# Kernel tuning notes

Hardware: AMD Instinct MI355X
Metric: run time of the kernel (lower is better)

The kernel has to match this reference:

```python
import jax, jax.numpy as jnp
import numpy as np

NUM_HEADS = 12


def setup_inputs() -> dict:
    key = jax.random.key(0)
    k_x, k_m, k_qkv, k_proj = jax.random.split(key, 4)
    B, N, C = 2, 2048, 768
    x = jax.random.normal(k_x, (B, N, C), dtype=jnp.float32)
    # binary key mask: 1 = attend, 0 = masked out
    mask = jax.random.randint(k_m, (B, N), 0, 2).astype(jnp.int32)
    # torch Linear(dim, dim*3, bias=False): stored here as [in, out]
    w_qkv = jax.random.normal(k_qkv, (C, 3 * C), dtype=jnp.float32) * 0.02
    w_proj = jax.random.normal(k_proj, (C, C), dtype=jnp.float32) * 0.02
    b_proj = jnp.zeros((C,), dtype=jnp.float32)
    return {"x": x, "mask": mask, "w_qkv": w_qkv, "w_proj": w_proj, "b_proj": b_proj}


def reference(x, mask, w_qkv, w_proj, b_proj):
    B, N, C = x.shape
    H = NUM_HEADS
    hd = C // H
    scale = hd ** -0.5
    qkv = (x @ w_qkv).reshape(B, N, 3, H, hd)
    q, k, v = jnp.moveaxis(qkv, 2, 0)            # each [B, N, H, hd]
    attn = jnp.einsum('bnhd,bmhd->bhnm', q, k) * scale  # [B, H, N, N]
    # faithful masked_softmax: unstable exp (no max subtraction), mask keys, renormalize
    m = mask.astype(x.dtype)[:, None, None, :]   # [B, 1, 1, N]
    x_exp = jnp.exp(attn) * m
    attn = x_exp / x_exp.sum(-1, keepdims=True)
    out = jnp.einsum('bhnm,bmhd->bnhd', attn, v).reshape(B, N, C)
    return out @ w_proj + b_proj
```

## Files before the change

### kernel.cpp

```cpp
#include <hip/hip_runtime.h>
#include <cstdint>

#define NB 2
#define NSEQ 2048
#define CDIM 768
#define NH 12
#define HD 64
#define NTOK (NB*NSEQ)
#define QKV_COLS (3*CDIM)
#define NBLK ((NSEQ/64)*NH*NB)

typedef short bf16x8 __attribute__((ext_vector_type(8)));
typedef short bf16x4 __attribute__((ext_vector_type(4)));
typedef float f32x4  __attribute__((ext_vector_type(4)));
typedef short short4v __attribute__((ext_vector_type(4)));
typedef unsigned int uint2v __attribute__((ext_vector_type(2)));
typedef unsigned int uint4v __attribute__((ext_vector_type(4)));

#define MFMA16(a,b,c) __builtin_amdgcn_mfma_f32_16x16x32_bf16(a,b,c,0,0,0)

__device__ __forceinline__ short f2b(float f) {
    uint32_t u = __builtin_bit_cast(uint32_t, f);
    u += 0x7fffu + ((u >> 16) & 1u);
    return (short)(u >> 16);
}
__device__ __forceinline__ unsigned pack2(float a, float b) {
    unsigned ua = __builtin_bit_cast(unsigned, a) + 0x7fffu;
    unsigned ub = __builtin_bit_cast(unsigned, b) + 0x7fffu;
    return __builtin_amdgcn_perm(ub, ua, 0x07060302u);
}
__device__ __forceinline__ void gll16(const short* g, short* l) {
    __builtin_amdgcn_global_load_lds(
        (const __attribute__((address_space(1))) unsigned int*)g,
        (__attribute__((address_space(3))) unsigned int*)l, 16, 0, 0);
}

__global__ __launch_bounds__(256) void prep_kernel(
    const float* __restrict__ x, const float* __restrict__ w_qkv,
    const float* __restrict__ w_proj,
    short* __restrict__ xb, short* __restrict__ wqt, short* __restrict__ wpt)
{
    __shared__ float tile[32][33];
    const int bid = blockIdx.x, t = threadIdx.x;
    if (bid < 3072) {
        int i = bid * 256 + t;
        float4 v = ((const float4*)x)[i];
        short4v o = { f2b(v.x), f2b(v.y), f2b(v.z), f2b(v.w) };
        ((short4v*)xb)[i] = o;
        return;
    }
    const float* w; short* wt; int K, NC, n0, k0;
    if (bid < 3072 + 1728) {
        int r = bid - 3072;
        w = w_qkv; wt = wqt; K = CDIM; NC = QKV_COLS;
        n0 = (r % 72) * 32; k0 = (r / 72) * 32;
    } else {
        int r = bid - 4800;
        w = w_proj; wt = wpt; K = CDIM; NC = CDIM;
        n0 = (r % 24) * 32; k0 = (r / 24) * 32;
    }
    #pragma unroll
    for (int i = 0; i < 4; ++i) {
        int idx = t + i * 256; int r = idx >> 5, c = idx & 31;
        tile[r][c] = w[(size_t)(k0 + r) * NC + n0 + c];
    }
    __syncthreads();
    #pragma unroll
    for (int i = 0; i < 4; ++i) {
        int idx = t + i * 256; int r = idx >> 5, c = idx & 31;
        wt[(size_t)(n0 + r) * K + k0 + c] = f2b(tile[c][r]);
    }
}

#define STAGEG(K0, B) do {                                                       \
    short* a_ = As + (B)*4096; short* b_ = Bs + (B)*4096;                        \
    gll16(ag0 + (K0), a_ + wid*512);                                             \
    gll16(ag1 + (K0), a_ + 2048 + wid*512);                                      \
    gll16(bg0 + (K0), b_ + wid*512);                                             \
    gll16(bg1 + (K0), b_ + 2048 + wid*512);                                      \
} while (0)

#define COMPUTEG(B) do {                                                         \
    const short* A_ = As + (B)*4096; const short* B_ = Bs + (B)*4096;            \
    bf16x8 af_[4], bf_[4];                                                       \
    _Pragma("unroll")                                                            \
    for (int i = 0; i < 4; ++i)                                                  \
        af_[i] = *(const bf16x8*)&A_[(wA*64 + i*16 + l16) * 32 + quad*8];        \
    _Pragma("unroll")                                                            \
    for (int j = 0; j < 4; ++j)                                                  \
        bf_[j] = *(const bf16x8*)&B_[(wB*64 + j*16 + l16) * 32 + quad*8];        \
    _Pragma("unroll")                                                            \
    for (int i = 0; i < 4; ++i)                                                  \
        _Pragma("unroll")                                                        \
        for (int j = 0; j < 4; ++j)                                              \
            acc[i][j] = MFMA16(af_[i], bf_[j], acc[i][j]);                       \
} while (0)

#define GEMM_LOOP() do {                                                         \
    STAGEG(0, 0); __syncthreads();                                               \
    for (int k0 = 0; k0 < CDIM; k0 += 64) {                                      \
        STAGEG(k0 + 32, 1);                                                      \
        COMPUTEG(0);                                                             \
        __syncthreads();                                                         \
        STAGEG((k0 + 64 < CDIM) ? k0 + 64 : 0, 0);                               \
        COMPUTEG(1);                                                             \
        __syncthreads();                                                         \
    }                                                                            \
} while (0)

__global__ __launch_bounds__(256) void gemm_qkv(
    const short* __restrict__ A ,
    const short* __restrict__ B ,
    short* __restrict__ qb, short* __restrict__ kb, short* __restrict__ vt)
{
    __shared__ short As[8192];
    __shared__ short Bs[8192];
    const int t = threadIdx.x;
    const int lane = t & 63, wid = t >> 6;
    const int quad = lane >> 4, l16 = lane & 15;
    const int wA = wid >> 1, wB = wid & 1;
    const int n0 = blockIdx.x * 128;
    const int m0 = blockIdx.y * 128;

    const int srow = wid * 16 + (lane >> 2), schunk = (lane & 3) * 8;
    const short* ag0 = A + (size_t)(n0 + srow) * CDIM + schunk;
    const short* ag1 = ag0 + (size_t)64 * CDIM;
    const short* bg0 = B + (size_t)(m0 + srow) * CDIM + schunk;
    const short* bg1 = bg0 + (size_t)64 * CDIM;

    f32x4 acc[4][4] = {};
    GEMM_LOOP();

    const int colbase = n0 + wA * 64;
    const int s = colbase / CDIM;
    const int h = (colbase - s * CDIM) >> 6;
    const int b = m0 >> 11;
    const size_t bh = (size_t)(b * NH + h);
    const float qsc = (s == 0) ? 0.125f : 1.0f;
    #pragma unroll
    for (int i = 0; i < 4; ++i) {
        const int d0 = i*16 + quad*4;
        #pragma unroll
        for (int j = 0; j < 4; ++j) {
            int tok = (m0 + wB*64 + j*16 + l16) & (NSEQ - 1);
            if (s < 2) {
                short* dst = (s == 0 ? qb : kb) + (bh * NSEQ + tok) * HD + d0;
                short4v o = { f2b(acc[i][j][0] * qsc), f2b(acc[i][j][1] * qsc),
                              f2b(acc[i][j][2] * qsc), f2b(acc[i][j][3] * qsc) };
                *(short4v*)dst = o;
            } else {
                short* dst = vt + (bh * HD + d0) * NSEQ + tok;
                #pragma unroll
                for (int r = 0; r < 4; ++r)
                    dst[(size_t)r * NSEQ] = f2b(acc[i][j][r]);
            }
        }
    }
}

#define STAGE64(KT, BUF) do {                                                    \
    short* kd_ = (BUF);                                                          \
    short* vd_ = (BUF) + 4096;                                                   \
    _Pragma("unroll")                                                            \
    for (int j = 0; j < 2; ++j) {                                                \
        gll16(kp + (size_t)((KT) + sRow[j]) * HD + sC[j]*8, kd_ + wid*1024 + j*512); \
        gll16(vp + (size_t)sRow[j] * NSEQ + (KT) + sC[j]*8, vd_ + wid*1024 + j*512); \
    }                                                                            \
} while (0)

#define BODY_S(KT, BUF, pP, vL) do {                                             \
    const short* Kb_ = (BUF);                                                    \
    const short* Vb_ = (BUF) + 4096;                                             \
    int4 mi_ = *(const int4*)(mp + (KT) + kbase);                                \
    bf16x8 kf0_ = *(const bf16x8*)&Kb_[krow64 + kc0];                            \
    bf16x8 kf1_ = *(const bf16x8*)&Kb_[krow64 + kc1];                            \
    f32x4 s_[4] = {};                                                            \
    _Pragma("unroll")                                                            \
    for (int jt = 0; jt < 4; ++jt) {                                             \
        s_[jt] = MFMA16(kf0_, qf[jt][0], s_[jt]);                                \
        s_[jt] = MFMA16(kf1_, qf[jt][1], s_[jt]);                                \
    }                                                                            \
    float4 m_ = {(float)mi_.x, (float)mi_.y, (float)mi_.z, (float)mi_.w};        \
    _Pragma("unroll")                                                            \
    for (int jt = 0; jt < 4; ++jt) {                                             \
        float e0 = __expf(s_[jt][0]) * m_.x;                                     \
        float e1 = __expf(s_[jt][1]) * m_.y;                                     \
        float e2 = __expf(s_[jt][2]) * m_.z;                                     \
        float e3 = __expf(s_[jt][3]) * m_.w;                                     \
        l[jt] += (e0 + e1) + (e2 + e3);                                          \
        pP[jt] = (uint2v){ pack2(e0, e1), pack2(e2, e3) };                       \
    }                                                                            \
    _Pragma("unroll")                                                            \
    for (int it = 0; it < 4; ++it)                                               \
        vL[it] = *(const bf16x4*)&Vb_[(it*16 + l16)*64 + vslot + vsub];          \
} while (0)

#define BODY_PV(pLo, vLo, pHi, vHi) do {                                         \
    bf16x8 pb_[4];                                                               \
    _Pragma("unroll")                                                            \
    for (int jt = 0; jt < 4; ++jt) {                                             \
        uint4v u_ = { pLo[jt].x, pLo[jt].y, pHi[jt].x, pHi[jt].y };              \
        pb_[jt] = __builtin_bit_cast(bf16x8, u_);                                \
    }                                                                            \
    _Pragma("unroll")                                                            \
    for (int it = 0; it < 4; ++it) {                                             \
        bf16x8 vf_ = __builtin_shufflevector(vLo[it], vHi[it], 0,1,2,3,4,5,6,7); \
        _Pragma("unroll")                                                        \
        for (int jt = 0; jt < 4; ++jt)                                           \
            o_acc[it][jt] = MFMA16(vf_, pb_[jt], o_acc[it][jt]);                 \
    }                                                                            \
} while (0)

__global__ __launch_bounds__(256) void attn_kernel(
    const short* __restrict__ qb, const short* __restrict__ kb,
    const short* __restrict__ vt, const int* __restrict__ mask,
    short* __restrict__ ao)
{
    __shared__ __align__(16) short KV2[2][8192];
    float (*Ob)[68] = (float(*)[68])KV2;
    float (*lsum)[64] = (float(*)[64])((char*)KV2 + 17408);

    const int t = threadIdx.x;
    const int lane = t & 63, wid = t >> 6;
    const int quad = lane >> 4, l16 = lane & 15;
    const int id = blockIdx.x;
    const int idx = id >> 3;
    const int bh = (id & 7) + ((idx % 3) << 3);
    const int q0 = (idx / 3) << 6;
    const int b = bh / NH, h = bh - b * NH;
    const size_t hoff = (size_t)bh * NSEQ * HD;
    const short* qp = qb + hoff;
    const short* kp = kb + hoff;
    const short* vp = vt + hoff;
    const int* mp = mask + b * NSEQ;
    const int kbase = wid * 16 + quad * 4;

    int sRow[2], sC[2];
    #pragma unroll
    for (int j = 0; j < 2; ++j) {
        sRow[j] = wid * 16 + j * 8 + (lane >> 3);
        sC[j]   = (lane & 7) ^ (sRow[j] & 7);
    }
    const int r7 = l16 & 7;
    const int krow64 = (wid * 16 + l16) * 64;
    const int kc0 = ((quad       ^ r7) << 3);
    const int kc1 = (((quad + 4) ^ r7) << 3);
    const int vslot = (((wid*2 + (quad >> 1)) ^ r7) << 3);
    const int vsub  = (quad & 1) * 4;

    bf16x8 qf[4][2];
    #pragma unroll
    for (int jt = 0; jt < 4; ++jt) {
        const short* qr = qp + (size_t)(q0 + jt*16 + l16) * HD + quad*8;
        qf[jt][0] = *(const bf16x8*)qr;
        qf[jt][1] = *(const bf16x8*)(qr + 32);
    }

    f32x4 o_acc[4][4] = {};
    float l[4] = {0.f, 0.f, 0.f, 0.f};
    uint2v pLo[4], pHi[4];
    bf16x4 vLo[4], vHi[4];

    STAGE64(0, KV2[0]);
    __syncthreads();

    for (int kt = 0; kt < NSEQ; kt += 128) {
        STAGE64(kt + 64, KV2[1]);
        BODY_S(kt, KV2[0], pLo, vLo);
        __syncthreads();
        STAGE64((kt + 128) & (NSEQ - 1), KV2[0]);
        BODY_S(kt + 64, KV2[1], pHi, vHi);
        BODY_PV(pLo, vLo, pHi, vHi);
        __syncthreads();
    }

    #pragma unroll
    for (int jt = 0; jt < 4; ++jt) {
        l[jt] += __shfl_xor(l[jt], 16);
        l[jt] += __shfl_xor(l[jt], 32);
        if (quad == 0) lsum[wid][jt*16 + l16] = l[jt];
    }
    for (int w = 0; w < 4; ++w) {
        __syncthreads();
        if (wid == w) {
            #pragma unroll
            for (int it = 0; it < 4; ++it)
                #pragma unroll
                for (int jt = 0; jt < 4; ++jt)
                    #pragma unroll
                    for (int r = 0; r < 4; ++r) {
                        if (w == 0)
                            Ob[it*16 + quad*4 + r][jt*16 + l16] = o_acc[it][jt][r];
                        else
                            Ob[it*16 + quad*4 + r][jt*16 + l16] += o_acc[it][jt][r];
                    }
        }
    }
    __syncthreads();

    {
        const int ql = t >> 2, dc = (t & 3) * 16;
        float inv = 1.0f / (((lsum[0][ql] + lsum[1][ql]) +
                             (lsum[2][ql] + lsum[3][ql])));
        bf16x8 o8a, o8b;
        #pragma unroll
        for (int d = 0; d < 8; ++d) o8a[d] = f2b(Ob[dc + d][ql] * inv);
        #pragma unroll
        for (int d = 0; d < 8; ++d) o8b[d] = f2b(Ob[dc + 8 + d][ql] * inv);
        int tok = b * NSEQ + q0 + ql;
        short* dst = ao + (size_t)tok * CDIM + h * HD + dc;
        *(bf16x8*)dst = o8a;
        *(bf16x8*)(dst + 8) = o8b;
    }
}

__global__ __launch_bounds__(256) void gemm_proj(
    const short* __restrict__ A ,
    const short* __restrict__ B ,
    const float* __restrict__ bias, float* __restrict__ out)
{
    __shared__ short As[8192];
    __shared__ short Bs[8192];
    const int t = threadIdx.x;
    const int lane = t & 63, wid = t >> 6;
    const int quad = lane >> 4, l16 = lane & 15;
    const int wA = wid >> 1, wB = wid & 1;
    const int n0 = blockIdx.x * 128;
    const int m0 = blockIdx.y * 128;

    const int srow = wid * 16 + (lane >> 2), schunk = (lane & 3) * 8;
    const short* ag0 = A + (size_t)(n0 + srow) * CDIM + schunk;
    const short* ag1 = ag0 + (size_t)64 * CDIM;
    const short* bg0 = B + (size_t)(m0 + srow) * CDIM + schunk;
    const short* bg1 = bg0 + (size_t)64 * CDIM;

    f32x4 acc[4][4] = {};
    GEMM_LOOP();

    #pragma unroll
    for (int i = 0; i < 4; ++i) {
        int col0 = n0 + wA*64 + i*16 + quad*4;
        float4 bias4 = *(const float4*)&bias[col0];
        #pragma unroll
        for (int j = 0; j < 4; ++j) {
            int tok = m0 + wB*64 + j*16 + l16;
            float4 o = { acc[i][j][0] + bias4.x, acc[i][j][1] + bias4.y,
                         acc[i][j][2] + bias4.z, acc[i][j][3] + bias4.w };
            *(float4*)(out + (size_t)tok * CDIM + col0) = o;
        }
    }
}

extern "C" void kernel_launch(void* const* d_in, const int* in_sizes, int n_in,
                              void* d_out, int out_size, void* d_ws, size_t ws_size,
                              hipStream_t stream)
{
    const float* x      = (const float*)d_in[0];
    const int*   mask   = (const int*)d_in[1];
    const float* w_qkv  = (const float*)d_in[2];
    const float* w_proj = (const float*)d_in[3];
    const float* b_proj = (const float*)d_in[4];
    float* out = (float*)d_out;

    const size_t SZ = (size_t)NTOK * CDIM;
    short* xb  = (short*)d_ws;
    short* wqt = xb  + SZ;
    short* wpt = wqt + (size_t)QKV_COLS * CDIM;
    short* qb  = wpt + (size_t)CDIM * CDIM;
    short* kb  = qb  + SZ;
    short* vt  = kb  + SZ;
    short* ao  = vt  + SZ;

    dim3 blk(256);
    prep_kernel<<<dim3(5376), blk, 0, stream>>>(x, w_qkv, w_proj, xb, wqt, wpt);
    gemm_qkv<<<dim3(QKV_COLS/128, NTOK/128), blk, 0, stream>>>(wqt, xb, qb, kb, vt);
    attn_kernel<<<dim3(NBLK), blk, 0, stream>>>(qb, kb, vt, mask, ao);
    gemm_proj<<<dim3(CDIM/128, NTOK/128), blk, 0, stream>>>(wpt, ao, b_proj, out);
}
```

Baseline: 181.3 us.

## Split attention over key halves with a reduce kernel; stage QKV epilogue through LDS

The attention kernel now splits each query tile's key range into two halves. This doubles the block count from 768 to 1536 to fill more CUs. Each half writes unnormalized fp32 partial outputs and row sums, and a new reduce kernel combines them and normalizes to bf16. Separately, the QKV GEMM epilogue transposes its tile through shared memory so Q/K/V stores become coalesced 16-byte writes instead of scattered short writes. The cost is extra fp32 partial traffic, an additional kernel launch, and an extra barrier in the GEMM epilogue.

```diff
diff --git a/kernel.cpp b/kernel.cpp
--- a/kernel.cpp
+++ b/kernel.cpp
@@ -8,7 +8,8 @@
 #define HD 64
 #define NTOK (NB*NSEQ)
 #define QKV_COLS (3*CDIM)
-#define NBLK ((NSEQ/64)*NH*NB)
+#define NBLK_ATTN (((NSEQ/64)*NH*NB)*2)
+#define NBLK_RED  ((NSEQ/64)*NH*NB)
 
 typedef short bf16x8 __attribute__((ext_vector_type(8)));
 typedef short bf16x4 __attribute__((ext_vector_type(4)));
@@ -113,8 +114,9 @@
     const short* __restrict__ B ,
     short* __restrict__ qb, short* __restrict__ kb, short* __restrict__ vt)
 {
-    __shared__ short As[8192];
-    __shared__ short Bs[8192];
+    __shared__ __align__(16) short SM[17408];
+    short* const As = SM;
+    short* const Bs = SM + 8192;
     const int t = threadIdx.x;
     const int lane = t & 63, wid = t >> 6;
     const int quad = lane >> 4, l16 = lane & 15;
@@ -131,30 +133,51 @@
     f32x4 acc[4][4] = {};
     GEMM_LOOP();
 
-    const int colbase = n0 + wA * 64;
-    const int s = colbase / CDIM;
-    const int h = (colbase - s * CDIM) >> 6;
-    const int b = m0 >> 11;
-    const size_t bh = (size_t)(b * NH + h);
+    const int s  = n0 / CDIM;
+    const int h0 = (n0 - s * CDIM) >> 6;
+    const int b  = m0 >> 11;
     const float qsc = (s == 0) ? 0.125f : 1.0f;
-    #pragma unroll
-    for (int i = 0; i < 4; ++i) {
-        const int d0 = i*16 + quad*4;
-        #pragma unroll
-        for (int j = 0; j < 4; ++j) {
-            int tok = (m0 + wB*64 + j*16 + l16) & (NSEQ - 1);
-            if (s < 2) {
-                short* dst = (s == 0 ? qb : kb) + (bh * NSEQ + tok) * HD + d0;
-                short4v o = { f2b(acc[i][j][0] * qsc), f2b(acc[i][j][1] * qsc),
-                              f2b(acc[i][j][2] * qsc), f2b(acc[i][j][3] * qsc) };
-                *(short4v*)dst = o;
-            } else {
-                short* dst = vt + (bh * HD + d0) * NSEQ + tok;
+    short* const CT = SM;
+
+    if (s < 2) {
+        #pragma unroll
+        for (int i = 0; i < 4; ++i)
+            #pragma unroll
+            for (int j = 0; j < 4; ++j) {
+                int tok = wB*64 + j*16 + l16;
+                int col = wA*64 + i*16 + quad*4;
+                short4v o = { f2b(acc[i][j][0]*qsc), f2b(acc[i][j][1]*qsc),
+                              f2b(acc[i][j][2]*qsc), f2b(acc[i][j][3]*qsc) };
+                *(short4v*)&CT[tok*136 + col] = o;
+            }
+        __syncthreads();
+        const int tok = t >> 1, hf = t & 1;
+        short* dst = (s == 0 ? qb : kb)
+                   + ((size_t)(b*NH + h0 + hf) * NSEQ + (m0 & 2047) + tok) * HD;
+        const short* src = &CT[tok*136 + hf*64];
+        #pragma unroll
+        for (int k = 0; k < 8; ++k)
+            *(float4*)(dst + k*8) = *(const float4*)(src + k*8);
+    } else {
+        #pragma unroll
+        for (int i = 0; i < 4; ++i)
+            #pragma unroll
+            for (int j = 0; j < 4; ++j) {
+                int tok = wB*64 + j*16 + l16;
+                int col = wA*64 + i*16 + quad*4;
                 #pragma unroll
                 for (int r = 0; r < 4; ++r)
-                    dst[(size_t)r * NSEQ] = f2b(acc[i][j][r]);
+                    CT[(col + r)*136 + tok] = f2b(acc[i][j][r]);
             }
-        }
+        __syncthreads();
+        const int row = t >> 1, hf = t & 1;
+        const int hh = h0 + (row >> 6), d = row & 63;
+        short* dst = vt + ((size_t)(b*NH + hh) * HD + d) * NSEQ
+                   + (m0 & 2047) + hf*64;
+        const short* src = &CT[row*136 + hf*64];
+        #pragma unroll
+        for (int k = 0; k < 8; ++k)
+            *(float4*)(dst + k*8) = *(const float4*)(src + k*8);
     }
 }
 
@@ -214,7 +237,7 @@
 __global__ __launch_bounds__(256) void attn_kernel(
     const short* __restrict__ qb, const short* __restrict__ kb,
     const short* __restrict__ vt, const int* __restrict__ mask,
-    short* __restrict__ ao)
+    float* __restrict__ opart, float* __restrict__ lpart)
 {
     __shared__ __align__(16) short KV2[2][8192];
     float (*Ob)[68] = (float(*)[68])KV2;
@@ -226,7 +249,10 @@
     const int id = blockIdx.x;
     const int idx = id >> 3;
     const int bh = (id & 7) + ((idx % 3) << 3);
-    const int q0 = (idx / 3) << 6;
+    const int rem = idx / 3;
+    const int q0 = (rem >> 1) << 6;
+    const int split = rem & 1;
+    const int koff = split << 10;
     const int b = bh / NH, h = bh - b * NH;
     const size_t hoff = (size_t)bh * NSEQ * HD;
     const short* qp = qb + hoff;
@@ -234,6 +260,7 @@
     const short* vp = vt + hoff;
     const int* mp = mask + b * NSEQ;
     const int kbase = wid * 16 + quad * 4;
+    const int slab = ((bh * 32 + (q0 >> 6)) << 1) + split;
 
     int sRow[2], sC[2];
     #pragma unroll
@@ -261,14 +288,14 @@
     uint2v pLo[4], pHi[4];
     bf16x4 vLo[4], vHi[4];
 
-    STAGE64(0, KV2[0]);
+    STAGE64(koff, KV2[0]);
     __syncthreads();
 
-    for (int kt = 0; kt < NSEQ; kt += 128) {
+    for (int kt = koff; kt < koff + 1024; kt += 128) {
         STAGE64(kt + 64, KV2[1]);
         BODY_S(kt, KV2[0], pLo, vLo);
         __syncthreads();
-        STAGE64((kt + 128) & (NSEQ - 1), KV2[0]);
+        STAGE64((kt + 128 < koff + 1024) ? kt + 128 : koff, KV2[0]);
         BODY_S(kt + 64, KV2[1], pHi, vHi);
         BODY_PV(pLo, vLo, pHi, vHi);
         __syncthreads();
@@ -300,18 +327,49 @@
 
     {
         const int ql = t >> 2, dc = (t & 3) * 16;
-        float inv = 1.0f / (((lsum[0][ql] + lsum[1][ql]) +
-                             (lsum[2][ql] + lsum[3][ql])));
-        bf16x8 o8a, o8b;
-        #pragma unroll
-        for (int d = 0; d < 8; ++d) o8a[d] = f2b(Ob[dc + d][ql] * inv);
-        #pragma unroll
-        for (int d = 0; d < 8; ++d) o8b[d] = f2b(Ob[dc + 8 + d][ql] * inv);
-        int tok = b * NSEQ + q0 + ql;
-        short* dst = ao + (size_t)tok * CDIM + h * HD + dc;
-        *(bf16x8*)dst = o8a;
-        *(bf16x8*)(dst + 8) = o8b;
-    }
+        float* po = opart + (size_t)slab * 4096 + ql * 64 + dc;
+        #pragma unroll
+        for (int k = 0; k < 4; ++k) {
+            float4 o4 = { Ob[dc + k*4 + 0][ql], Ob[dc + k*4 + 1][ql],
+                          Ob[dc + k*4 + 2][ql], Ob[dc + k*4 + 3][ql] };
+            *(float4*)(po + k*4) = o4;
+        }
+        if (t < 64)
+            lpart[(size_t)slab * 64 + t] =
+                ((lsum[0][t] + lsum[1][t]) + (lsum[2][t] + lsum[3][t]));
+    }
+}
+
+__global__ __launch_bounds__(256) void attn_reduce(
+    const float* __restrict__ opart, const float* __restrict__ lpart,
+    short* __restrict__ ao)
+{
+    const int id = blockIdx.x, t = threadIdx.x;
+    const int xcd = id & 7, g = id >> 3;
+    const int qt = g & 31, bhhi = g >> 5;
+    const int bh = xcd + (bhhi << 3);
+    const int b = bh / NH, h = bh - b * NH;
+    const int slab0 = (bh * 32 + qt) << 1;
+    const int ql = t >> 2, dc = (t & 3) << 4;
+    const float* p0 = opart + (size_t)slab0 * 4096 + ql * 64 + dc;
+    const float* p1 = p0 + 4096;
+    const float inv = 1.0f /
+        (lpart[(size_t)slab0 * 64 + ql] + lpart[(size_t)(slab0 + 1) * 64 + ql]);
+    bf16x8 oa, ob;
+    #pragma unroll
+    for (int k = 0; k < 2; ++k) {
+        float4 a0 = ((const float4*)p0)[k*2],     a1 = ((const float4*)p0)[k*2+1];
+        float4 c0 = ((const float4*)p1)[k*2],     c1 = ((const float4*)p1)[k*2+1];
+        bf16x8 o8;
+        o8[0] = f2b((a0.x + c0.x) * inv); o8[1] = f2b((a0.y + c0.y) * inv);
+        o8[2] = f2b((a0.z + c0.z) * inv); o8[3] = f2b((a0.w + c0.w) * inv);
+        o8[4] = f2b((a1.x + c1.x) * inv); o8[5] = f2b((a1.y + c1.y) * inv);
+        o8[6] = f2b((a1.z + c1.z) * inv); o8[7] = f2b((a1.w + c1.w) * inv);
+        if (k == 0) oa = o8; else ob = o8;
+    }
+    short* dst = ao + ((size_t)(b * NSEQ + qt * 64 + ql)) * CDIM + h * HD + dc;
+    *(bf16x8*)dst = oa;
+    *(bf16x8*)(dst + 8) = ob;
 }
 
 __global__ __launch_bounds__(256) void gemm_proj(
@@ -319,8 +377,9 @@
     const short* __restrict__ B ,
     const float* __restrict__ bias, float* __restrict__ out)
 {
-    __shared__ short As[8192];
-    __shared__ short Bs[8192];
+    __shared__ short SMp[16384];
+    short* const As = SMp;
+    short* const Bs = SMp + 8192;
     const int t = threadIdx.x;
     const int lane = t & 63, wid = t >> 6;
     const int quad = lane >> 4, l16 = lane & 15;
@@ -370,10 +429,13 @@
     short* kb  = qb  + SZ;
     short* vt  = kb  + SZ;
     short* ao  = vt  + SZ;
+    float* opart = (float*)(ao + SZ);
+    float* lpart = opart + (size_t)NBLK_ATTN * 4096;
 
     dim3 blk(256);
     prep_kernel<<<dim3(5376), blk, 0, stream>>>(x, w_qkv, w_proj, xb, wqt, wpt);
     gemm_qkv<<<dim3(QKV_COLS/128, NTOK/128), blk, 0, stream>>>(wqt, xb, qb, kb, vt);
-    attn_kernel<<<dim3(NBLK), blk, 0, stream>>>(qb, kb, vt, mask, ao);
+    attn_kernel<<<dim3(NBLK_ATTN), blk, 0, stream>>>(qb, kb, vt, mask, opart, lpart);
+    attn_reduce<<<dim3(NBLK_RED), blk, 0, stream>>>(opart, lpart, ao);
     gemm_proj<<<dim3(CDIM/128, NTOK/128), blk, 0, stream>>>(wpt, ao, b_proj, out);
 }
```

New measurement: 185.8 us. 1.02x slower.
